# Optimization experiments

Measured on AMD Instinct MI355X. Metric: run time of the kernel, lower is better.

The kernel has to match this reference:

```python
import jax, jax.numpy as jnp
import numpy as np

B, L, D = 2, 2048, 2048
N, K, H = 16, 8, 128
EPS = 1e-6
ROPE_THETA = 1000000
K_MASK = -2.3819763e+38


def rms_norm(x, w, eps=EPS):
    dtype = x.dtype
    rms = jnp.sqrt(jnp.mean(x.astype(jnp.float32) ** 2, axis=-1, keepdims=True) + eps)
    return (w * x / rms).astype(dtype)


def apply_rope(inputs, positions, head_dim, rope_theta=ROPE_THETA):
    # inputs: [B, L, n, H], positions: [B, L]
    fraction = 2 * jnp.arange(0, head_dim // 2, dtype=jnp.float32) / head_dim
    timescale = rope_theta ** fraction  # [H/2]
    sinusoid = positions[..., jnp.newaxis] / timescale[jnp.newaxis, jnp.newaxis, :]  # [B,L,H/2]
    sinusoid = sinusoid[..., jnp.newaxis, :]  # [B,L,1,H/2]
    sin, cos = jnp.sin(sinusoid), jnp.cos(sinusoid)
    first, second = jnp.split(inputs, 2, axis=-1)
    out = jnp.concatenate([first * cos - second * sin, second * cos + first * sin], axis=-1)
    return out.astype(inputs.dtype)


def setup_inputs() -> dict:
    key = jax.random.key(0)
    ks = jax.random.split(key, 6)
    x = jax.random.normal(ks[0], (B, L, D), dtype=jnp.float32)
    position_ids = jnp.broadcast_to(jnp.arange(L, dtype=jnp.int32)[None, :], (B, L))
    # causal mask [B, L, S]
    attn_mask = jnp.broadcast_to(jnp.tril(jnp.ones((L, L), dtype=bool))[None], (B, L, L))
    wq = jax.random.normal(ks[1], (D, N, H), dtype=jnp.float32) * 0.02
    wk = jax.random.normal(ks[2], (D, K, H), dtype=jnp.float32) * 0.02
    wv = jax.random.normal(ks[3], (D, K, H), dtype=jnp.float32) * 0.02
    wo = jax.random.normal(ks[4], (N, H, D), dtype=jnp.float32) * 0.02
    q_norm_w = jnp.ones((H,), dtype=jnp.float32)
    k_norm_w = jnp.ones((H,), dtype=jnp.float32)
    return {"x": x, "position_ids": position_ids, "attn_mask": attn_mask,
            "wq": wq, "wk": wk, "wv": wv, "wo": wo,
            "q_norm_w": q_norm_w, "k_norm_w": k_norm_w}


def reference(x, position_ids, attn_mask, wq, wk, wv, wo, q_norm_w, k_norm_w):
    scale = H ** (-0.5)
    q = jnp.einsum('BLD,DNH->BLNH', x, wq)  # [B,L,N,H]
    k = jnp.einsum('BSD,DKH->BSKH', x, wk)  # [B,S,K,H]
    v = jnp.einsum('BSD,DKH->BSKH', x, wv)
    q = rms_norm(q, q_norm_w)
    k = rms_norm(k, k_norm_w)
    q = apply_rope(q, position_ids, H)
    k = apply_rope(k, position_ids, H)
    b, l, n, h = q.shape
    s = k.shape[1]
    kk = k.shape[2]
    q = q.reshape((b, l, kk, n // kk, h))
    attn = jnp.einsum('BLKGH,BSKH->BKGLS', q, k) * scale
    attn = attn.reshape((b, n, l, s))
    attn = jnp.where(jnp.expand_dims(attn_mask, -3), attn, K_MASK)
    attn = jax.nn.softmax(attn.astype(jnp.float32), axis=-1).astype(k.dtype)
    attn = attn.reshape((b, kk, n // kk, l, s))
    qkv = jnp.einsum('BKGLS,BSKH->BLKGH', attn, v).reshape((b, l, n, h))
    out = jnp.einsum('BLNH,NHD->BLD', qkv, wo)
    return out
```

## Files before the change

kernel.cpp:

```cpp
#include <hip/hip_runtime.h>

#define B_ 2
#define L_ 2048
#define D_ 2048
#define NH_ 16
#define KH_ 8
#define HD_ 128

typedef __attribute__((ext_vector_type(8))) short short8;
typedef __attribute__((ext_vector_type(4))) short short4v;
typedef __attribute__((ext_vector_type(4))) float floatx4;

__device__ __forceinline__ unsigned short f2bf(float f) {
  unsigned u = __float_as_uint(f);
  unsigned r = (u + 0x7fffu + ((u >> 16) & 1u)) >> 16;
  return (unsigned short)r;
}
__device__ __forceinline__ float bf2f(unsigned short h) {
  return __uint_as_float(((unsigned)h) << 16);
}
__device__ __forceinline__ void gl_lds16(const void* g, void* l) {
  __builtin_amdgcn_global_load_lds(
      (const __attribute__((address_space(1))) unsigned int*)g,
      (__attribute__((address_space(3))) unsigned int*)l, 16, 0, 0);
}

__global__ __launch_bounds__(256) void prep1(const float* __restrict__ x,
                                             const float* __restrict__ wq,
                                             const float* __restrict__ wk,
                                             const float* __restrict__ wv,
                                             const float* __restrict__ wo,
                                             unsigned short* __restrict__ xb,
                                             unsigned short* __restrict__ wqkv_t,
                                             unsigned short* __restrict__ wo_t) {
  int id = blockIdx.x;
  int t = threadIdx.x;
  if (id < 8192) {
    long i = ((long)id * 256 + t) * 4;
    float4 v = *(const float4*)(x + i);
    ushort4 o;
    o.x = f2bf(v.x); o.y = f2bf(v.y); o.z = f2bf(v.z); o.w = f2bf(v.w);
    *(ushort4*)(xb + i) = o;
    return;
  }
  id -= 8192;
  __shared__ float tile[32][33];
  const float* in;
  unsigned short* out;
  int C, sh;
  if (id < 4096) {
    in = wq; out = wqkv_t; C = 2048; sh = 6;
  } else if (id < 6144) {
    in = wk; out = wqkv_t + 2048L * 2048; C = 1024; sh = 5; id -= 4096;
  } else if (id < 8192) {
    in = wv; out = wqkv_t + 3072L * 2048; C = 1024; sh = 5; id -= 6144;
  } else {
    in = wo; out = wo_t; C = 2048; sh = 6; id -= 8192;
  }
  int c0 = (id & ((1 << sh) - 1)) * 32, r0 = (id >> sh) * 32;
  int tx = t & 31, ty = t >> 5;
#pragma unroll
  for (int i = 0; i < 4; i++)
    tile[ty + i * 8][tx] = in[(long)(r0 + ty + i * 8) * C + c0 + tx];
  __syncthreads();
#pragma unroll
  for (int i = 0; i < 4; i++) {
    int oc = ty + i * 8;
    out[(long)(c0 + oc) * 2048 + r0 + tx] = f2bf(tile[tx][oc]);
  }
}

__global__ __launch_bounds__(256) void prep2(const unsigned short* __restrict__ qkv,
                                             const int* __restrict__ pos,
                                             const float* __restrict__ qw,
                                             const float* __restrict__ kw,
                                             unsigned short* __restrict__ qo,
                                             unsigned short* __restrict__ ko,
                                             unsigned short* __restrict__ vT) {
  int id = blockIdx.x;
  int t = threadIdx.x;
  if (id < 24576) {
    const int lane = t & 63, w = t >> 6;
    const int gid = id * 4 + w;
    const int row = gid / 24;
    const int hd = gid - row * 24;
    const int b = row >> 11, l = row & 2047;
    const unsigned short* src = qkv + (long)row * 4096 + hd * 128;
    float x0 = bf2f(src[lane]);
    float x1 = bf2f(src[lane + 64]);
    float ss = x0 * x0 + x1 * x1;
#pragma unroll
    for (int off = 32; off; off >>= 1) ss += __shfl_xor(ss, off);
    float inv = 1.0f / sqrtf(ss * (1.0f / 128.0f) + 1e-6f);
    const float* nw = (hd < 16) ? qw : kw;
    x0 = nw[lane] * x0 * inv;
    x1 = nw[lane + 64] * x1 * inv;
    float p = (float)pos[row];
    float ang = p * exp2f((float)lane * -0.31143075889f);
    float s, c;
    sincosf(ang, &s, &c);
    float o0 = x0 * c - x1 * s;
    float o1 = x1 * c + x0 * s;
    unsigned short* dst;
    if (hd < 16) {
      const float QSC = 0.08838834764831845f * 1.4426950408889634f;
      o0 *= QSC;
      o1 *= QSC;
      dst = qo + (((long)b * NH_ + hd) * L_ + l) * HD_;
    } else {
      dst = ko + (((long)b * KH_ + (hd - 16)) * L_ + l) * HD_;
    }
    dst[lane] = f2bf(o0);
    dst[lane + 64] = f2bf(o1);
    return;
  }
  id -= 24576;
  __shared__ unsigned short tile[32][33];
  int l0 = (id & 63) * 32, h0 = ((id >> 6) & 3) * 32;
  int bk = id >> 8;
  int b = bk >> 3, kh = bk & 7;
  int tx = t & 31, ty = t >> 5;
  const unsigned short* src = qkv + (long)b * L_ * 4096 + 3072 + kh * 128;
#pragma unroll
  for (int i = 0; i < 4; i++)
    tile[ty + i * 8][tx] = src[(long)(l0 + ty + i * 8) * 4096 + h0 + tx];
  __syncthreads();
  unsigned short* dst = vT + (long)bk * HD_ * L_;
#pragma unroll
  for (int i = 0; i < 4; i++)
    dst[(long)(h0 + ty + i * 8) * L_ + l0 + tx] = tile[tx][ty + i * 8];
}

template <int MODE>
__global__ __launch_bounds__(256, 3) void gemm128(const unsigned short* __restrict__ A,
                                                  const unsigned short* __restrict__ Bt,
                                                  void* __restrict__ C,
                                                  int M, int N, int K) {
  __shared__ unsigned short As[128 * 64];
  __shared__ unsigned short Bs[128 * 64];
  const int t = threadIdx.x;
  const int lane = t & 63, w = t >> 6;
  const int wy = w >> 1, wx = w & 1;
  const int col = lane & 15, quad = lane >> 4;
  const long m0 = (long)blockIdx.y * 128, n0 = (long)blockIdx.x * 128;
  const int kbeg = (MODE == 2) ? blockIdx.z * (K >> 1) : 0;
  const int kend = (MODE == 2) ? kbeg + (K >> 1) : K;
  floatx4 acc[4][4];
#pragma unroll
  for (int i = 0; i < 4; i++)
#pragma unroll
    for (int j = 0; j < 4; j++) acc[i][j] = (floatx4)0.0f;
  const int rs = t >> 3, bs = t & 7;
  for (int kt = kbeg; kt < kend; kt += 64) {
#pragma unroll
    for (int i = 0; i < 4; i++) {
      int r = i * 32 + rs;
      gl_lds16(A + (m0 + r) * (long)K + kt + ((bs ^ (r & 7)) << 3),
               &As[(i * 32 + w * 8) * 64]);
      gl_lds16(Bt + (n0 + r) * (long)K + kt + ((bs ^ (r & 7)) << 3),
               &Bs[(i * 32 + w * 8) * 64]);
    }
    __syncthreads();
#pragma unroll
    for (int ks = 0; ks < 2; ks++) {
      short8 af[4], bf[4];
#pragma unroll
      for (int mi = 0; mi < 4; mi++) {
        int row = wy * 64 + mi * 16 + col;
        int blk = ks * 4 + quad;
        af[mi] = *(const short8*)&As[row * 64 + ((blk ^ (row & 7)) << 3)];
      }
#pragma unroll
      for (int ni = 0; ni < 4; ni++) {
        int row = wx * 64 + ni * 16 + col;
        int blk = ks * 4 + quad;
        bf[ni] = *(const short8*)&Bs[row * 64 + ((blk ^ (row & 7)) << 3)];
      }
#pragma unroll
      for (int mi = 0; mi < 4; mi++)
#pragma unroll
        for (int ni = 0; ni < 4; ni++)
          acc[mi][ni] = __builtin_amdgcn_mfma_f32_16x16x32_bf16(af[mi], bf[ni],
                                                                acc[mi][ni], 0, 0, 0);
    }
    __syncthreads();
  }
#pragma unroll
  for (int mi = 0; mi < 4; mi++)
#pragma unroll
    for (int r = 0; r < 4; r++) {
      long row = m0 + wy * 64 + mi * 16 + quad * 4 + r;
#pragma unroll
      for (int ni = 0; ni < 4; ni++) {
        long cg = n0 + wx * 64 + ni * 16 + col;
        float val = acc[mi][ni][r];
        if (MODE == 1)
          ((unsigned short*)C)[row * N + cg] = f2bf(val);
        else
          unsafeAtomicAdd(&((float*)C)[row * N + cg], val);
      }
    }
}

__global__ __launch_bounds__(256, 2) void flash(const unsigned short* __restrict__ Q,
                                                const unsigned short* __restrict__ Kg,
                                                const unsigned short* __restrict__ VT,
                                                unsigned short* __restrict__ Og) {
  __shared__ unsigned short Ks[64 * 128];
  __shared__ unsigned short Vs[128 * 64];
  __shared__ unsigned short Ps[128 * 72];
  const int n = blockIdx.y, b = blockIdx.z;
  const int qt = b ? (15 - blockIdx.x) : blockIdx.x;
  const int t = threadIdx.x, lane = t & 63, w = t >> 6;
  const int col = lane & 15, quad = lane >> 4;
  const int kvh = n >> 1;
  const unsigned short* kb = Kg + ((long)b * KH_ + kvh) * L_ * HD_;
  const unsigned short* vtb = VT + ((long)b * KH_ + kvh) * HD_ * L_;
  const int l0 = qt * 128;
  const int steps = 2 * qt + 2;
  const unsigned short* qb = Q + (((long)b * NH_ + n) * L_ + l0) * HD_;

  short8 qf[2][4];
#pragma unroll
  for (int mi = 0; mi < 2; mi++)
#pragma unroll
    for (int ks = 0; ks < 4; ks++)
      qf[mi][ks] = *(const short8*)(qb + (w * 32 + mi * 16 + col) * 128 + ks * 32 + quad * 8);

  floatx4 o[2][8];
#pragma unroll
  for (int mi = 0; mi < 2; mi++)
#pragma unroll
    for (int nf = 0; nf < 8; nf++) o[mi][nf] = (floatx4)0.0f;
  float lrow[2] = {0.0f, 0.0f};

  for (int st = 0; st < steps; st++) {
    const int s0 = st * 64;
    {
      const int rK = t >> 4, blkK = t & 15;
#pragma unroll
      for (int i = 0; i < 4; i++) {
        int r = i * 16 + rK;
        int gblk = (blkK & 8) | ((blkK ^ r) & 7);
        gl_lds16(kb + (long)(s0 + r) * 128 + gblk * 8, &Ks[(i * 16 + w * 4) * 128]);
      }
    }
    {
      const int rV = t >> 3, blkV = t & 7;
#pragma unroll
      for (int j = 0; j < 4; j++) {
        int r = j * 32 + rV;
        int gblk = (blkV ^ r) & 7;
        gl_lds16(vtb + (long)r * L_ + s0 + gblk * 8, &Vs[(j * 32 + w * 8) * 64]);
      }
    }
    __syncthreads();

    floatx4 sa[2][4];
#pragma unroll
    for (int mi = 0; mi < 2; mi++)
#pragma unroll
      for (int sf = 0; sf < 4; sf++) sa[mi][sf] = (floatx4)0.0f;
#pragma unroll
    for (int ks = 0; ks < 4; ks++) {
      short8 bf[4];
#pragma unroll
      for (int sf = 0; sf < 4; sf++) {
        int srow = sf * 16 + col;
        int blk = ks * 4 + quad;
        bf[sf] = *(const short8*)&Ks[srow * 128 + (((blk & 8) | ((blk ^ srow) & 7)) << 3)];
      }
#pragma unroll
      for (int mi = 0; mi < 2; mi++)
#pragma unroll
        for (int sf = 0; sf < 4; sf++)
          sa[mi][sf] = __builtin_amdgcn_mfma_f32_16x16x32_bf16(bf[sf], qf[mi][ks],
                                                               sa[mi][sf], 0, 0, 0);
    }

    if (st >= steps - 2) {
#pragma unroll
      for (int mi = 0; mi < 2; mi++) {
        int lg = l0 + w * 32 + mi * 16 + col;
#pragma unroll
        for (int sf = 0; sf < 4; sf++)
#pragma unroll
          for (int r = 0; r < 4; r++) {
            int sg = s0 + sf * 16 + quad * 4 + r;
            if (sg > lg) sa[mi][sf][r] = -3.0e38f;
          }
      }
    }

#pragma unroll
    for (int mi = 0; mi < 2; mi++)
#pragma unroll
      for (int sf = 0; sf < 4; sf++) {
        short4v pk;
#pragma unroll
        for (int r = 0; r < 4; r++) {
          float pv = exp2f(sa[mi][sf][r] - 17.0f);
          lrow[mi] += pv;
          pk[r] = (short)f2bf(pv);
        }
        *(short4v*)&Ps[(w * 32 + mi * 16 + col) * 72 + sf * 16 + quad * 4] = pk;
      }

#pragma unroll
    for (int ks = 0; ks < 2; ks++) {
      short8 pf[2];
#pragma unroll
      for (int mi = 0; mi < 2; mi++)
        pf[mi] = *(const short8*)&Ps[(w * 32 + mi * 16 + col) * 72 + ks * 32 + quad * 8];
      short8 vf[8];
#pragma unroll
      for (int nf = 0; nf < 8; nf++) {
        int h = nf * 16 + col;
        int blk = ks * 4 + quad;
        vf[nf] = *(const short8*)&Vs[h * 64 + ((blk ^ (h & 7)) << 3)];
      }
#pragma unroll
      for (int mi = 0; mi < 2; mi++)
#pragma unroll
        for (int nf = 0; nf < 8; nf++)
          o[mi][nf] = __builtin_amdgcn_mfma_f32_16x16x32_bf16(pf[mi], vf[nf],
                                                              o[mi][nf], 0, 0, 0);
    }
    __syncthreads();
  }

#pragma unroll
  for (int mi = 0; mi < 2; mi++) {
    float s = lrow[mi];
    s += __shfl_xor(s, 16);
    s += __shfl_xor(s, 32);
#pragma unroll
    for (int r = 0; r < 4; r++) {
      float inv = 1.0f / __shfl(s, quad * 4 + r);
      int lg = l0 + w * 32 + mi * 16 + quad * 4 + r;
      unsigned short* dst = Og + (((long)b * L_ + lg) * NH_ + n) * HD_;
#pragma unroll
      for (int nf = 0; nf < 8; nf++)
        dst[nf * 16 + col] = f2bf(o[mi][nf][r] * inv);
    }
  }
}

extern "C" void kernel_launch(void* const* d_in, const int* in_sizes, int n_in,
                              void* d_out, int out_size, void* d_ws, size_t ws_size,
                              hipStream_t stream) {
  const float* x = (const float*)d_in[0];
  const int* pos = (const int*)d_in[1];
  const float* wq = (const float*)d_in[3];
  const float* wk = (const float*)d_in[4];
  const float* wv = (const float*)d_in[5];
  const float* wo = (const float*)d_in[6];
  const float* qnw = (const float*)d_in[7];
  const float* knw = (const float*)d_in[8];
  float* out = (float*)d_out;

  char* ws = (char*)d_ws;
  unsigned short* xb     = (unsigned short*)(ws + 0);
  unsigned short* wqkv_t = (unsigned short*)(ws + 16777216);
  unsigned short* wo_t   = (unsigned short*)(ws + 33554432);
  unsigned short* qkv    = (unsigned short*)(ws + 41943040);
  unsigned short* q      = (unsigned short*)(ws + 75497472);
  unsigned short* k      = (unsigned short*)(ws + 92274688);
  unsigned short* vT     = (unsigned short*)(ws + 100663296);
  unsigned short* ao     = (unsigned short*)(ws + 109051904);
  if (ws_size < 125829120) return;

  hipMemsetAsync(d_out, 0, (size_t)out_size * 4, stream);
  prep1<<<20480, 256, 0, stream>>>(x, wq, wk, wv, wo, xb, wqkv_t, wo_t);
  gemm128<1><<<dim3(32, 32), 256, 0, stream>>>(xb, wqkv_t, qkv, 4096, 4096, 2048);
  prep2<<<28672, 256, 0, stream>>>(qkv, pos, qnw, knw, q, k, vT);
  flash<<<dim3(16, NH_, B_), 256, 0, stream>>>(q, k, vT, ao);
  gemm128<2><<<dim3(16, 32, 2), 256, 0, stream>>>(ao, wo_t, out, 4096, 2048, 2048);
}
```

Measured before the change: 382.6 us.

## Prefetch next K/V tile into registers in flash attention; drop split-K output GEMM

The flash kernel now loads the first K/V tile directly into LDS. Each later tile is prefetched from global memory into registers while the current tile is computed, then written to LDS between two LDS-only barriers. This is meant to hide global load latency behind the MFMA work. Separately, the output projection drops split-K with atomic adds and the output memset, and uses a single full-K GEMM with plain stores. That removes atomic traffic and one memset but halves the output GEMM grid (512 blocks) and raises register pressure in flash.

```diff
diff --git a/kernel.cpp b/kernel.cpp
--- a/kernel.cpp
+++ b/kernel.cpp
@@ -23,6 +23,10 @@
   __builtin_amdgcn_global_load_lds(
       (const __attribute__((address_space(1))) unsigned int*)g,
       (__attribute__((address_space(3))) unsigned int*)l, 16, 0, 0);
+}
+__device__ __forceinline__ void barrier_lds_only() {
+  asm volatile("s_waitcnt lgkmcnt(0)" ::: "memory");
+  __builtin_amdgcn_s_barrier();
 }
 
 __global__ __launch_bounds__(256) void prep1(const float* __restrict__ x,
@@ -143,15 +147,13 @@
   const int wy = w >> 1, wx = w & 1;
   const int col = lane & 15, quad = lane >> 4;
   const long m0 = (long)blockIdx.y * 128, n0 = (long)blockIdx.x * 128;
-  const int kbeg = (MODE == 2) ? blockIdx.z * (K >> 1) : 0;
-  const int kend = (MODE == 2) ? kbeg + (K >> 1) : K;
   floatx4 acc[4][4];
 #pragma unroll
   for (int i = 0; i < 4; i++)
 #pragma unroll
     for (int j = 0; j < 4; j++) acc[i][j] = (floatx4)0.0f;
   const int rs = t >> 3, bs = t & 7;
-  for (int kt = kbeg; kt < kend; kt += 64) {
+  for (int kt = 0; kt < K; kt += 64) {
 #pragma unroll
     for (int i = 0; i < 4; i++) {
       int r = i * 32 + rs;
@@ -197,7 +199,7 @@
         if (MODE == 1)
           ((unsigned short*)C)[row * N + cg] = f2bf(val);
         else
-          unsafeAtomicAdd(&((float*)C)[row * N + cg], val);
+          ((float*)C)[row * N + cg] = val;
       }
     }
 }
@@ -220,6 +222,9 @@
   const int steps = 2 * qt + 2;
   const unsigned short* qb = Q + (((long)b * NH_ + n) * L_ + l0) * HD_;
 
+  const int rK = t >> 4, blkK = t & 15;
+  const int rV = t >> 3, blkV = t & 7;
+
   short8 qf[2][4];
 #pragma unroll
   for (int mi = 0; mi < 2; mi++)
@@ -234,27 +239,41 @@
     for (int nf = 0; nf < 8; nf++) o[mi][nf] = (floatx4)0.0f;
   float lrow[2] = {0.0f, 0.0f};
 
+  {
+#pragma unroll
+    for (int i = 0; i < 4; i++) {
+      int r = i * 16 + rK;
+      int gblk = (blkK & 8) | ((blkK ^ r) & 7);
+      gl_lds16(kb + (long)r * 128 + gblk * 8, &Ks[(i * 16 + w * 4) * 128]);
+    }
+#pragma unroll
+    for (int j = 0; j < 4; j++) {
+      int r = j * 32 + rV;
+      int gblk = (blkV ^ r) & 7;
+      gl_lds16(vtb + (long)r * L_ + gblk * 8, &Vs[(j * 32 + w * 8) * 64]);
+    }
+  }
+  __syncthreads();
+
+  short8 kpre[4], vpre[4];
+  if (steps > 1) {
+    const int s0n = 64;
+#pragma unroll
+    for (int i = 0; i < 4; i++) {
+      int r = i * 16 + rK;
+      int gblk = (blkK & 8) | ((blkK ^ r) & 7);
+      kpre[i] = *(const short8*)(kb + (long)(s0n + r) * 128 + gblk * 8);
+    }
+#pragma unroll
+    for (int j = 0; j < 4; j++) {
+      int r = j * 32 + rV;
+      int gblk = (blkV ^ r) & 7;
+      vpre[j] = *(const short8*)(vtb + (long)r * L_ + s0n + gblk * 8);
+    }
+  }
+
   for (int st = 0; st < steps; st++) {
     const int s0 = st * 64;
-    {
-      const int rK = t >> 4, blkK = t & 15;
-#pragma unroll
-      for (int i = 0; i < 4; i++) {
-        int r = i * 16 + rK;
-        int gblk = (blkK & 8) | ((blkK ^ r) & 7);
-        gl_lds16(kb + (long)(s0 + r) * 128 + gblk * 8, &Ks[(i * 16 + w * 4) * 128]);
-      }
-    }
-    {
-      const int rV = t >> 3, blkV = t & 7;
-#pragma unroll
-      for (int j = 0; j < 4; j++) {
-        int r = j * 32 + rV;
-        int gblk = (blkV ^ r) & 7;
-        gl_lds16(vtb + (long)r * L_ + s0 + gblk * 8, &Vs[(j * 32 + w * 8) * 64]);
-      }
-    }
-    __syncthreads();
 
     floatx4 sa[2][4];
 #pragma unroll
@@ -326,7 +345,36 @@
           o[mi][nf] = __builtin_amdgcn_mfma_f32_16x16x32_bf16(pf[mi], vf[nf],
                                                               o[mi][nf], 0, 0, 0);
     }
-    __syncthreads();
+
+    barrier_lds_only();
+    if (st + 1 < steps) {
+#pragma unroll
+      for (int i = 0; i < 4; i++) {
+        int r = i * 16 + rK;
+        *(short8*)&Ks[r * 128 + blkK * 8] = kpre[i];
+      }
+#pragma unroll
+      for (int j = 0; j < 4; j++) {
+        int r = j * 32 + rV;
+        *(short8*)&Vs[r * 64 + blkV * 8] = vpre[j];
+      }
+      barrier_lds_only();
+      if (st + 2 < steps) {
+        const int s0n = (st + 2) * 64;
+#pragma unroll
+        for (int i = 0; i < 4; i++) {
+          int r = i * 16 + rK;
+          int gblk = (blkK & 8) | ((blkK ^ r) & 7);
+          kpre[i] = *(const short8*)(kb + (long)(s0n + r) * 128 + gblk * 8);
+        }
+#pragma unroll
+        for (int j = 0; j < 4; j++) {
+          int r = j * 32 + rV;
+          int gblk = (blkV ^ r) & 7;
+          vpre[j] = *(const short8*)(vtb + (long)r * L_ + s0n + gblk * 8);
+        }
+      }
+    }
   }
 
 #pragma unroll
@@ -370,10 +418,9 @@
   unsigned short* ao     = (unsigned short*)(ws + 109051904);
   if (ws_size < 125829120) return;
 
-  hipMemsetAsync(d_out, 0, (size_t)out_size * 4, stream);
   prep1<<<20480, 256, 0, stream>>>(x, wq, wk, wv, wo, xb, wqkv_t, wo_t);
   gemm128<1><<<dim3(32, 32), 256, 0, stream>>>(xb, wqkv_t, qkv, 4096, 4096, 2048);
   prep2<<<28672, 256, 0, stream>>>(qkv, pos, qnw, knw, q, k, vT);
   flash<<<dim3(16, NH_, B_), 256, 0, stream>>>(q, k, vT, ao);
-  gemm128<2><<<dim3(16, 32, 2), 256, 0, stream>>>(ao, wo_t, out, 4096, 2048, 2048);
-}
+  gemm128<0><<<dim3(16, 32), 256, 0, stream>>>(ao, wo_t, out, 4096, 2048, 2048);
+}
```

Result: faster. 361.8 us (-5.5%).
